# Optimization experiments

Measured on AMD Instinct MI355X. Metric: run time of the kernel, lower is better.

Reference implementation:

```python
import jax, jax.numpy as jnp
import numpy as np

N = 100000
E = 1600000
IN_FEATS = 512
N_HIDDEN = 128
N_CLASSES = 40


def setup_inputs() -> dict:
    key = jax.random.key(0)
    k1, k2, k3, k4, k5, k6, k7 = jax.random.split(key, 7)
    inputs = jax.random.normal(k1, (N, IN_FEATS), dtype=jnp.float32)
    edge_index = jax.random.randint(k2, (2, E), 0, N, dtype=jnp.int64)
    edge_attr = jax.random.uniform(k3, (E,), dtype=jnp.float32)
    # GCNConv params (Glorot-ish scaling)
    W1 = jax.random.normal(k4, (IN_FEATS, N_HIDDEN), dtype=jnp.float32) / np.sqrt(IN_FEATS)
    b1 = jnp.zeros((N_HIDDEN,), dtype=jnp.float32)
    W2 = jax.random.normal(k5, (N_HIDDEN, N_CLASSES), dtype=jnp.float32) / np.sqrt(N_HIDDEN)
    b2 = jnp.zeros((N_CLASSES,), dtype=jnp.float32)
    return {"inputs": inputs, "edge_index": edge_index, "edge_attr": edge_attr,
            "W1": W1, "b1": b1, "W2": W2, "b2": b2}


def gcn_conv(x, W, b, src, dst, edge_weight):
    """GCNConv with normalize=False: linear transform, then edge-weighted
    scatter-sum from src to dst, then bias."""
    m = x @ W                                   # [N, F_out]
    msgs = m[src] * edge_weight[:, None]        # gather + weight, [E, F_out]
    agg = jax.ops.segment_sum(msgs, dst, num_segments=x.shape[0])  # scatter-add
    return agg + b


def reference(inputs, edge_index, edge_attr, W1, b1, W2, b2):
    src, dst = edge_index[0], edge_index[1]
    h = jax.nn.relu(gcn_conv(inputs, W1, b1, src, dst, edge_attr))
    # F.dropout with training=False (eval mode) is identity -> deterministic baseline
    preds = gcn_conv(h, W2, b2, src, dst, edge_attr)
    return jax.nn.log_softmax(preds, axis=1)
```

## Files before the change

kernel.cpp:

```cpp
#include <hip/hip_runtime.h>
#include <hip/hip_bf16.h>
#include <cstdint>

#define N_NODES 100000
#define N_EDGES 1600000
#define F_IN    512
#define F_HID   128
#define F_OUT   40
#define F_OUT_PAD 48

#define BSH    8
#define NB     391
#define BEPT   8
#define BCHUNK 4096
#define GB     391
#define FCAP   6144

typedef short v8s __attribute__((ext_vector_type(8)));
typedef float v4f __attribute__((ext_vector_type(4)));

__device__ __forceinline__ short f2bf(float f) {
    unsigned u = __float_as_uint(f);
    u += 0x7fffu + ((u >> 16) & 1u);
    return (short)(u >> 16);
}

__device__ __forceinline__ v8s pack8(float4 a, float4 b) {
    v8s r;
    r[0] = f2bf(a.x); r[1] = f2bf(a.y); r[2] = f2bf(a.z); r[3] = f2bf(a.w);
    r[4] = f2bf(b.x); r[5] = f2bf(b.y); r[6] = f2bf(b.z); r[7] = f2bf(b.w);
    return r;
}

__device__ __forceinline__ void gload16(const void* g, void* l) {
    __builtin_amdgcn_global_load_lds(
        (const __attribute__((address_space(1))) void*)g,
        (__attribute__((address_space(3))) void*)l, 16, 0, 0);
}


__global__ __launch_bounds__(512) void k_bhist(const int* __restrict__ dst,
                                               int* __restrict__ bcnt) {
    __shared__ int lh[512];
    int tid = threadIdx.x;
    lh[tid] = 0;
    __syncthreads();
    long e0 = (long)blockIdx.x * BCHUNK;
#pragma unroll
    for (int i = 0; i < BEPT; i++) {
        long e = e0 + tid + i * 512;
        if (e < N_EDGES) atomicAdd(&lh[dst[e] >> BSH], 1);
    }
    __syncthreads();
    if (tid < NB && lh[tid]) atomicAdd(&bcnt[tid], lh[tid]);
}

__global__ __launch_bounds__(512) void k_bscan(const int* __restrict__ bcnt,
                                               int* __restrict__ bbase,
                                               int* __restrict__ bcur) {
    __shared__ int sm[512];
    int tid = threadIdx.x;
    int v = (tid < NB) ? bcnt[tid] : 0;
    sm[tid] = v;
    __syncthreads();
    for (int off = 1; off < 512; off <<= 1) {
        int t = (tid >= off) ? sm[tid - off] : 0;
        __syncthreads();
        sm[tid] += t;
        __syncthreads();
    }
    if (tid < NB) {
        int ex = sm[tid] - v;
        bbase[tid] = ex;
        bcur[tid] = ex;
    }
    if (tid == 511) bbase[NB] = sm[511];
}

__global__ __launch_bounds__(512) void k_bscatter(const int* __restrict__ src,
                                                  const int* __restrict__ dst,
                                                  const float* __restrict__ w,
                                                  int* __restrict__ bcur,
                                                  int2* __restrict__ tmp) {
    __shared__ int cntA[512];
    __shared__ int ofsA[512];
    __shared__ int lcur[512];
    __shared__ int gb[512];
    __shared__ __align__(16) int2 recBuf[BCHUNK];
    __shared__ unsigned short bkt[BCHUNK];
    int tid = threadIdx.x;
    long e0 = (long)blockIdx.x * BCHUNK;
    cntA[tid] = 0;
    __syncthreads();

    int dloc[BEPT];
#pragma unroll
    for (int i = 0; i < BEPT; i++) {
        long e = e0 + tid + i * 512;
        int d = (e < N_EDGES) ? dst[e] : -1;
        dloc[i] = d;
        if (d >= 0) atomicAdd(&cntA[d >> BSH], 1);
    }
    __syncthreads();

    int v = cntA[tid];
    ofsA[tid] = v;
    __syncthreads();
    for (int off = 1; off < 512; off <<= 1) {
        int t = (tid >= off) ? ofsA[tid - off] : 0;
        __syncthreads();
        ofsA[tid] += t;
        __syncthreads();
    }
    int excl = ofsA[tid] - v;
    ofsA[tid] = excl;
    lcur[tid] = excl;
    if (tid < NB && v > 0) gb[tid] = atomicAdd(&bcur[tid], v);
    __syncthreads();

#pragma unroll
    for (int i = 0; i < BEPT; i++) {
        int d = dloc[i];
        if (d >= 0) {
            long e = e0 + tid + i * 512;
            int j = d >> BSH;
            int slot = atomicAdd(&lcur[j], 1);
            recBuf[slot] = make_int2(src[e] | ((d & 255) << 17), __float_as_int(w[e]));
            bkt[slot] = (unsigned short)j;
        }
    }
    __syncthreads();

    long rem = N_EDGES - e0;
    int total = (rem < BCHUNK) ? (int)rem : BCHUNK;
    for (int s = tid; s < total; s += 512) {
        int j = bkt[s];
        tmp[gb[j] + (s - ofsA[j])] = recBuf[s];
    }
}

__global__ __launch_bounds__(256) void k_fine(const int2* __restrict__ tmp,
                                              const int* __restrict__ bbase,
                                              int2* __restrict__ rec,
                                              int* __restrict__ rowptr,
                                              int* __restrict__ deg) {
    __shared__ int hist[256];
    __shared__ int ofs[256];
    __shared__ int cur[256];
    __shared__ __align__(16) int2 recOut[FCAP];
    int tid = threadIdx.x, b = blockIdx.x;
    int base = bbase[b];
    int cnt = bbase[b + 1] - base;

    hist[tid] = 0;
    __syncthreads();
    for (int i = tid; i < cnt; i += 256) {
        unsigned u = (unsigned)tmp[base + i].x;
        atomicAdd(&hist[u >> 17], 1);
    }
    __syncthreads();

    int v = hist[tid];
    ofs[tid] = v;
    __syncthreads();
    for (int off = 1; off < 256; off <<= 1) {
        int t = (tid >= off) ? ofs[tid - off] : 0;
        __syncthreads();
        ofs[tid] += t;
        __syncthreads();
    }
    int excl = ofs[tid] - v;
    ofs[tid] = excl;
    cur[tid] = excl;
    int node = (b << BSH) + tid;
    if (node < N_NODES) {
        rowptr[node] = base + excl;
        deg[node] = v;
    }
    __syncthreads();

    if (cnt <= FCAP) {
        for (int i = tid; i < cnt; i += 256) {
            int2 r = tmp[base + i];
            unsigned u = (unsigned)r.x;
            int slot = atomicAdd(&cur[u >> 17], 1);
            recOut[slot] = make_int2((int)(u & 0x1FFFFu), r.y);
        }
        __syncthreads();
        for (int i = tid; i < cnt; i += 256) rec[base + i] = recOut[i];
    } else {
        for (int i = tid; i < cnt; i += 256) {
            int2 r = tmp[base + i];
            unsigned u = (unsigned)r.x;
            int slot = atomicAdd(&cur[u >> 17], 1);
            rec[base + slot] = make_int2((int)(u & 0x1FFFFu), r.y);
        }
    }
}


__global__ void k_convW(const float* __restrict__ W1, short* __restrict__ WT1,
                        const float* __restrict__ W2, short* __restrict__ WT2) {
    int i = blockIdx.x * blockDim.x + threadIdx.x;
    if (i < F_IN * F_HID) {
        int n = i >> 9, k = i & 511;
        WT1[i] = f2bf(W1[k * F_HID + n]);
    } else {
        int j = i - F_IN * F_HID;
        if (j < F_OUT_PAD * F_HID) {
            int n = j >> 7, k = j & 127;
            WT2[j] = (n < F_OUT) ? f2bf(W2[k * F_OUT + n]) : (short)0;
        }
    }
}


__global__ __launch_bounds__(256) void k_gemm1(const float* __restrict__ x,
                                               const short* __restrict__ WT1,
                                               unsigned short* __restrict__ m1b) {
    __shared__ __align__(16) float aBuf[2][64 * 32];
    __shared__ __align__(16) short bBuf[2][128 * 32];
    int tid = threadIdx.x, w = tid >> 6, lane = tid & 63;
    int quad = lane >> 4, l16 = lane & 15;
    long rowBase = (long)blockIdx.x * 64;

    int ar = lane >> 3, ac = lane & 7;
    int br = lane >> 2, bc = lane & 3;

    v4f acc[8];
#pragma unroll
    for (int t = 0; t < 8; t++) acc[t] = (v4f){0.f, 0.f, 0.f, 0.f};

    auto stage = [&](int kc, int buf) {
#pragma unroll
        for (int i = 0; i < 2; i++) {
            int rl = w * 16 + i * 8 + ar;
            long rg = rowBase + rl;
            if (rg > N_NODES - 1) rg = N_NODES - 1;
            const float* gp = x + rg * F_IN + kc * 32 + ((ac ^ (rl & 7)) << 2);
            gload16(gp, &aBuf[buf][(w * 16 + i * 8) * 32]);
        }
#pragma unroll
        for (int i = 0; i < 2; i++) {
            int n = w * 32 + i * 16 + br;
            const short* gp = WT1 + n * F_IN + kc * 32 + ((bc ^ ((n >> 1) & 3)) << 3);
            gload16(gp, &bBuf[buf][(w * 32 + i * 16) * 32]);
        }
    };

    stage(0, 0);
#pragma unroll
    for (int kc = 0; kc < 16; kc++) {
        __syncthreads();
        int buf = kc & 1;
        if (kc < 15) stage(kc + 1, buf ^ 1);
        int arow = w * 16 + l16;
        int p0 = (2 * quad) ^ (l16 & 7);
        float4 av0 = *(const float4*)&aBuf[buf][arow * 32 + p0 * 4];
        float4 av1 = *(const float4*)&aBuf[buf][arow * 32 + (p0 ^ 1) * 4];
        v8s af = pack8(av0, av1);
#pragma unroll
        for (int t = 0; t < 8; t++) {
            int n = t * 16 + l16;
            int p = quad ^ ((n >> 1) & 3);
            v8s bf = *(const v8s*)&bBuf[buf][n * 32 + p * 8];
            acc[t] = __builtin_amdgcn_mfma_f32_16x16x32_bf16(af, bf, acc[t], 0, 0, 0);
        }
    }

#pragma unroll
    for (int t = 0; t < 8; t++)
#pragma unroll
        for (int r = 0; r < 4; r++) {
            long row = rowBase + w * 16 + quad * 4 + r;
            if (row < N_NODES)
                m1b[row * F_HID + t * 16 + l16] = (unsigned short)f2bf(acc[t][r]);
        }
}


__global__ void k_agg1(const int2* __restrict__ rec, const int* __restrict__ rowptr,
                       const int* __restrict__ deg, const unsigned* __restrict__ m1u,
                       const float* __restrict__ b1, unsigned* __restrict__ h) {
    int node = blockIdx.x * 4 + (threadIdx.x >> 6);
    int lane = threadIdx.x & 63;
    if (node >= N_NODES) return;
    int start = rowptr[node], cnt = deg[node];

    float ax0 = 0.f, ay0 = 0.f, ax1 = 0.f, ay1 = 0.f;
    float ax2 = 0.f, ay2 = 0.f, ax3 = 0.f, ay3 = 0.f;
    int i = 0;
    for (; i + 4 <= cnt; i += 4) {
        int2 r0 = rec[start + i + 0];
        int2 r1 = rec[start + i + 1];
        int2 r2 = rec[start + i + 2];
        int2 r3 = rec[start + i + 3];
        unsigned u0 = m1u[(long)r0.x * 64 + lane];
        unsigned u1 = m1u[(long)r1.x * 64 + lane];
        unsigned u2 = m1u[(long)r2.x * 64 + lane];
        unsigned u3 = m1u[(long)r3.x * 64 + lane];
        float w0 = __int_as_float(r0.y), w1 = __int_as_float(r1.y);
        float w2 = __int_as_float(r2.y), w3 = __int_as_float(r3.y);
        ax0 = fmaf(w0, __uint_as_float(u0 << 16), ax0);
        ay0 = fmaf(w0, __uint_as_float(u0 & 0xffff0000u), ay0);
        ax1 = fmaf(w1, __uint_as_float(u1 << 16), ax1);
        ay1 = fmaf(w1, __uint_as_float(u1 & 0xffff0000u), ay1);
        ax2 = fmaf(w2, __uint_as_float(u2 << 16), ax2);
        ay2 = fmaf(w2, __uint_as_float(u2 & 0xffff0000u), ay2);
        ax3 = fmaf(w3, __uint_as_float(u3 << 16), ax3);
        ay3 = fmaf(w3, __uint_as_float(u3 & 0xffff0000u), ay3);
    }
    for (; i < cnt; i++) {
        int2 r = rec[start + i];
        unsigned u = m1u[(long)r.x * 64 + lane];
        float w = __int_as_float(r.y);
        ax0 = fmaf(w, __uint_as_float(u << 16), ax0);
        ay0 = fmaf(w, __uint_as_float(u & 0xffff0000u), ay0);
    }
    float accx = (ax0 + ax1) + (ax2 + ax3) + b1[2 * lane];
    float accy = (ay0 + ay1) + (ay2 + ay3) + b1[2 * lane + 1];
    accx = fmaxf(accx, 0.f);
    accy = fmaxf(accy, 0.f);
    unsigned packed = (unsigned)(unsigned short)f2bf(accx) |
                      ((unsigned)(unsigned short)f2bf(accy) << 16);
    h[(long)node * 64 + lane] = packed;
}


__global__ __launch_bounds__(256) void k_gemm2(const unsigned short* __restrict__ h,
                                               const short* __restrict__ WT2,
                                               unsigned short* __restrict__ m2b) {
    int wave = threadIdx.x >> 6, lane = threadIdx.x & 63;
    int quad = lane >> 4, l16 = lane & 15;
    long rowBase = ((long)blockIdx.x * 4 + wave) * 16;
    if (rowBase >= N_NODES) return;

    v4f acc[3];
#pragma unroll
    for (int t = 0; t < 3; t++) acc[t] = (v4f){0.f, 0.f, 0.f, 0.f};

    const short* arow = (const short*)h + (rowBase + l16) * (long)F_HID + quad * 8;
    const short* brow = WT2 + l16 * F_HID + quad * 8;
#pragma unroll
    for (int k0 = 0; k0 < F_HID; k0 += 32) {
        v8s af = *reinterpret_cast<const v8s*>(arow + k0);
#pragma unroll
        for (int t = 0; t < 3; t++) {
            v8s bf = *reinterpret_cast<const v8s*>(brow + t * 16 * F_HID + k0);
            acc[t] = __builtin_amdgcn_mfma_f32_16x16x32_bf16(af, bf, acc[t], 0, 0, 0);
        }
    }
#pragma unroll
    for (int r = 0; r < 4; r++) {
        long row = rowBase + quad * 4 + r;
#pragma unroll
        for (int t = 0; t < 3; t++)
            m2b[row * 64 + t * 16 + l16] = (unsigned short)f2bf(acc[t][r]);
        m2b[row * 64 + 48 + l16] = 0;
    }
}


__global__ void k_agg2(const int2* __restrict__ rec, const int* __restrict__ rowptr,
                       const int* __restrict__ deg, const unsigned short* __restrict__ m2b,
                       const float* __restrict__ b2, float* __restrict__ out) {
    int node = blockIdx.x * 4 + (threadIdx.x >> 6);
    int lane = threadIdx.x & 63;
    if (node >= N_NODES) return;
    int start = rowptr[node], cnt = deg[node];

    float a0 = 0.f, a1 = 0.f, a2 = 0.f, a3 = 0.f;
    int i = 0;
    for (; i + 4 <= cnt; i += 4) {
        int2 r0 = rec[start + i + 0];
        int2 r1 = rec[start + i + 1];
        int2 r2 = rec[start + i + 2];
        int2 r3 = rec[start + i + 3];
        unsigned short u0 = m2b[(long)r0.x * 64 + lane];
        unsigned short u1 = m2b[(long)r1.x * 64 + lane];
        unsigned short u2 = m2b[(long)r2.x * 64 + lane];
        unsigned short u3 = m2b[(long)r3.x * 64 + lane];
        a0 = fmaf(__int_as_float(r0.y), __uint_as_float((unsigned)u0 << 16), a0);
        a1 = fmaf(__int_as_float(r1.y), __uint_as_float((unsigned)u1 << 16), a1);
        a2 = fmaf(__int_as_float(r2.y), __uint_as_float((unsigned)u2 << 16), a2);
        a3 = fmaf(__int_as_float(r3.y), __uint_as_float((unsigned)u3 << 16), a3);
    }
    for (; i < cnt; i++) {
        int2 r = rec[start + i];
        unsigned short u = m2b[(long)r.x * 64 + lane];
        a0 = fmaf(__int_as_float(r.y), __uint_as_float((unsigned)u << 16), a0);
    }
    float acc = (a0 + a1) + (a2 + a3);
    if (lane < F_OUT) acc += b2[lane];
    float p = (lane < F_OUT) ? acc : -3.4e38f;
#pragma unroll
    for (int off = 32; off; off >>= 1) p = fmaxf(p, __shfl_xor(p, off));
    float ex = (lane < F_OUT) ? __expf(acc - p) : 0.f;
    float s = ex;
#pragma unroll
    for (int off = 32; off; off >>= 1) s += __shfl_xor(s, off);
    if (lane < F_OUT) out[(long)node * F_OUT + lane] = acc - p - __logf(s);
}


extern "C" void kernel_launch(void* const* d_in, const int* in_sizes, int n_in,
                              void* d_out, int out_size, void* d_ws, size_t ws_size,
                              hipStream_t stream) {
    const float* x  = (const float*)d_in[0];
    const int* ei   = (const int*)d_in[1];
    const int* src  = ei;
    const int* dst  = ei + N_EDGES;
    const float* ew = (const float*)d_in[2];
    const float* W1 = (const float*)d_in[3];
    const float* b1 = (const float*)d_in[4];
    const float* W2 = (const float*)d_in[5];
    const float* b2 = (const float*)d_in[6];
    float* out = (float*)d_out;

    char* ws = (char*)d_ws;
    size_t off = 0;
    auto alloc = [&](size_t bytes) {
        void* p = ws + off;
        off += (bytes + 255) & ~(size_t)255;
        return p;
    };
    unsigned short* m1b  = (unsigned short*)alloc((size_t)N_NODES * F_HID * 2);
    unsigned int*   h    = (unsigned int*)alloc((size_t)N_NODES * F_HID * 2);
    unsigned short* m2b  = (unsigned short*)alloc((size_t)N_NODES * 64 * 2);
    int2*           rec  = (int2*)alloc((size_t)N_EDGES * 8);
    int*          rowptr = (int*)alloc((size_t)N_NODES * 4);
    int*          deg    = (int*)alloc((size_t)N_NODES * 4);
    int*          bCnt   = (int*)alloc(512 * 4);
    int*          bBase  = (int*)alloc(512 * 4);
    int*          bCur   = (int*)alloc(512 * 4);
    short*        WT1    = (short*)alloc((size_t)F_HID * F_IN * 2);
    short*        WT2    = (short*)alloc((size_t)F_OUT_PAD * F_HID * 2);

    int2* tmp = (int2*)m2b;

    hipMemsetAsync(bCnt, 0, 512 * 4, stream);

    int convTot = F_IN * F_HID + F_OUT_PAD * F_HID;
    k_convW<<<(convTot + 255) / 256, 256, 0, stream>>>(W1, WT1, W2, WT2);

    k_bhist<<<GB, 512, 0, stream>>>(dst, bCnt);
    k_bscan<<<1, 512, 0, stream>>>(bCnt, bBase, bCur);
    k_bscatter<<<GB, 512, 0, stream>>>(src, dst, ew, bCur, tmp);
    k_fine<<<NB, 256, 0, stream>>>(tmp, bBase, rec, rowptr, deg);

    k_gemm1<<<(N_NODES + 63) / 64, 256, 0, stream>>>(x, WT1, m1b);
    k_agg1<<<(N_NODES + 3) / 4, 256, 0, stream>>>(rec, rowptr, deg, (const unsigned*)m1b, b1, h);
    k_gemm2<<<(N_NODES + 63) / 64, 256, 0, stream>>>((const unsigned short*)h, WT2, m2b);
    k_agg2<<<(N_NODES + 3) / 4, 256, 0, stream>>>(rec, rowptr, deg, m2b, b2, out);
}
```

Measured before the change: 523.1 us.

## Split aggregation wavefronts across edges with wider gathers and fuse weight conversion

```diff
diff --git a/kernel.cpp b/kernel.cpp
--- a/kernel.cpp
+++ b/kernel.cpp
@@ -14,6 +14,7 @@
 #define BEPT   8
 #define BCHUNK 4096
 #define GB     391
+#define CONVB  140
 #define FCAP   6144
 
 typedef short v8s __attribute__((ext_vector_type(8)));
@@ -24,6 +25,9 @@
     u += 0x7fffu + ((u >> 16) & 1u);
     return (short)(u >> 16);
 }
+
+__device__ __forceinline__ float bflo(unsigned u) { return __uint_as_float(u << 16); }
+__device__ __forceinline__ float bfhi(unsigned u) { return __uint_as_float(u & 0xffff0000u); }
 
 __device__ __forceinline__ v8s pack8(float4 a, float4 b) {
     v8s r;
@@ -40,7 +44,25 @@
 
 
 __global__ __launch_bounds__(512) void k_bhist(const int* __restrict__ dst,
-                                               int* __restrict__ bcnt) {
+                                               int* __restrict__ bcnt,
+                                               const float* __restrict__ W1,
+                                               short* __restrict__ WT1,
+                                               const float* __restrict__ W2,
+                                               short* __restrict__ WT2) {
+    if (blockIdx.x >= GB) {
+        int i = (blockIdx.x - GB) * 512 + threadIdx.x;
+        if (i < F_IN * F_HID) {
+            int n = i >> 9, k = i & 511;
+            WT1[i] = f2bf(W1[k * F_HID + n]);
+        } else {
+            int j = i - F_IN * F_HID;
+            if (j < F_OUT_PAD * F_HID) {
+                int n = j >> 7, k = j & 127;
+                WT2[j] = (n < F_OUT) ? f2bf(W2[k * F_OUT + n]) : (short)0;
+            }
+        }
+        return;
+    }
     __shared__ int lh[512];
     int tid = threadIdx.x;
     lh[tid] = 0;
@@ -199,22 +221,6 @@
 }
 
 
-__global__ void k_convW(const float* __restrict__ W1, short* __restrict__ WT1,
-                        const float* __restrict__ W2, short* __restrict__ WT2) {
-    int i = blockIdx.x * blockDim.x + threadIdx.x;
-    if (i < F_IN * F_HID) {
-        int n = i >> 9, k = i & 511;
-        WT1[i] = f2bf(W1[k * F_HID + n]);
-    } else {
-        int j = i - F_IN * F_HID;
-        if (j < F_OUT_PAD * F_HID) {
-            int n = j >> 7, k = j & 127;
-            WT2[j] = (n < F_OUT) ? f2bf(W2[k * F_OUT + n]) : (short)0;
-        }
-    }
-}
-
-
 __global__ __launch_bounds__(256) void k_gemm1(const float* __restrict__ x,
                                                const short* __restrict__ WT1,
                                                unsigned short* __restrict__ m1b) {
@@ -280,50 +286,64 @@
 
 
 __global__ void k_agg1(const int2* __restrict__ rec, const int* __restrict__ rowptr,
-                       const int* __restrict__ deg, const unsigned* __restrict__ m1u,
-                       const float* __restrict__ b1, unsigned* __restrict__ h) {
+                       const int* __restrict__ deg, const uint2* __restrict__ m1v,
+                       const float* __restrict__ b1, uint2* __restrict__ h2) {
     int node = blockIdx.x * 4 + (threadIdx.x >> 6);
     int lane = threadIdx.x & 63;
     if (node >= N_NODES) return;
+    int half = lane >> 5, l32 = lane & 31;
     int start = rowptr[node], cnt = deg[node];
 
-    float ax0 = 0.f, ay0 = 0.f, ax1 = 0.f, ay1 = 0.f;
-    float ax2 = 0.f, ay2 = 0.f, ax3 = 0.f, ay3 = 0.f;
-    int i = 0;
-    for (; i + 4 <= cnt; i += 4) {
-        int2 r0 = rec[start + i + 0];
-        int2 r1 = rec[start + i + 1];
-        int2 r2 = rec[start + i + 2];
-        int2 r3 = rec[start + i + 3];
-        unsigned u0 = m1u[(long)r0.x * 64 + lane];
-        unsigned u1 = m1u[(long)r1.x * 64 + lane];
-        unsigned u2 = m1u[(long)r2.x * 64 + lane];
-        unsigned u3 = m1u[(long)r3.x * 64 + lane];
+    float a0 = 0.f, a1 = 0.f, a2 = 0.f, a3 = 0.f;
+    float c0 = 0.f, c1 = 0.f, c2 = 0.f, c3 = 0.f;
+
+    int nmain = cnt >> 3;
+    int ebase = start + half;
+    for (int k = 0; k < nmain; k++) {
+        int e = ebase + (k << 3);
+        int2 r0 = rec[e];
+        int2 r1 = rec[e + 2];
+        int2 r2 = rec[e + 4];
+        int2 r3 = rec[e + 6];
+        uint2 g0 = m1v[(long)r0.x * 32 + l32];
+        uint2 g1 = m1v[(long)r1.x * 32 + l32];
+        uint2 g2 = m1v[(long)r2.x * 32 + l32];
+        uint2 g3 = m1v[(long)r3.x * 32 + l32];
         float w0 = __int_as_float(r0.y), w1 = __int_as_float(r1.y);
         float w2 = __int_as_float(r2.y), w3 = __int_as_float(r3.y);
-        ax0 = fmaf(w0, __uint_as_float(u0 << 16), ax0);
-        ay0 = fmaf(w0, __uint_as_float(u0 & 0xffff0000u), ay0);
-        ax1 = fmaf(w1, __uint_as_float(u1 << 16), ax1);
-        ay1 = fmaf(w1, __uint_as_float(u1 & 0xffff0000u), ay1);
-        ax2 = fmaf(w2, __uint_as_float(u2 << 16), ax2);
-        ay2 = fmaf(w2, __uint_as_float(u2 & 0xffff0000u), ay2);
-        ax3 = fmaf(w3, __uint_as_float(u3 << 16), ax3);
-        ay3 = fmaf(w3, __uint_as_float(u3 & 0xffff0000u), ay3);
-    }
-    for (; i < cnt; i++) {
-        int2 r = rec[start + i];
-        unsigned u = m1u[(long)r.x * 64 + lane];
+        a0 = fmaf(w0, bflo(g0.x), a0); a1 = fmaf(w0, bfhi(g0.x), a1);
+        a2 = fmaf(w0, bflo(g0.y), a2); a3 = fmaf(w0, bfhi(g0.y), a3);
+        c0 = fmaf(w1, bflo(g1.x), c0); c1 = fmaf(w1, bfhi(g1.x), c1);
+        c2 = fmaf(w1, bflo(g1.y), c2); c3 = fmaf(w1, bfhi(g1.y), c3);
+        a0 = fmaf(w2, bflo(g2.x), a0); a1 = fmaf(w2, bfhi(g2.x), a1);
+        a2 = fmaf(w2, bflo(g2.y), a2); a3 = fmaf(w2, bfhi(g2.y), a3);
+        c0 = fmaf(w3, bflo(g3.x), c0); c1 = fmaf(w3, bfhi(g3.x), c1);
+        c2 = fmaf(w3, bflo(g3.y), c2); c3 = fmaf(w3, bfhi(g3.y), c3);
+    }
+    for (int e = start + (nmain << 3) + half; e < start + cnt; e += 2) {
+        int2 r = rec[e];
+        uint2 g = m1v[(long)r.x * 32 + l32];
         float w = __int_as_float(r.y);
-        ax0 = fmaf(w, __uint_as_float(u << 16), ax0);
-        ay0 = fmaf(w, __uint_as_float(u & 0xffff0000u), ay0);
-    }
-    float accx = (ax0 + ax1) + (ax2 + ax3) + b1[2 * lane];
-    float accy = (ay0 + ay1) + (ay2 + ay3) + b1[2 * lane + 1];
-    accx = fmaxf(accx, 0.f);
-    accy = fmaxf(accy, 0.f);
-    unsigned packed = (unsigned)(unsigned short)f2bf(accx) |
-                      ((unsigned)(unsigned short)f2bf(accy) << 16);
-    h[(long)node * 64 + lane] = packed;
+        a0 = fmaf(w, bflo(g.x), a0); a1 = fmaf(w, bfhi(g.x), a1);
+        a2 = fmaf(w, bflo(g.y), a2); a3 = fmaf(w, bfhi(g.y), a3);
+    }
+    a0 += c0; a1 += c1; a2 += c2; a3 += c3;
+    a0 += __shfl_xor(a0, 32);
+    a1 += __shfl_xor(a1, 32);
+    a2 += __shfl_xor(a2, 32);
+    a3 += __shfl_xor(a3, 32);
+    if (half == 0) {
+        float4 bv = ((const float4*)b1)[l32];
+        a0 = fmaxf(a0 + bv.x, 0.f);
+        a1 = fmaxf(a1 + bv.y, 0.f);
+        a2 = fmaxf(a2 + bv.z, 0.f);
+        a3 = fmaxf(a3 + bv.w, 0.f);
+        unsigned lo = (unsigned)(unsigned short)f2bf(a0) |
+                      ((unsigned)(unsigned short)f2bf(a1) << 16);
+        unsigned hi = (unsigned)(unsigned short)f2bf(a2) |
+                      ((unsigned)(unsigned short)f2bf(a3) << 16);
+        h2[(long)node * 32 + l32] = make_uint2(lo, hi);
+    }
 }
 
 
@@ -362,44 +382,64 @@
 
 
 __global__ void k_agg2(const int2* __restrict__ rec, const int* __restrict__ rowptr,
-                       const int* __restrict__ deg, const unsigned short* __restrict__ m2b,
+                       const int* __restrict__ deg, const uint2* __restrict__ m2v,
                        const float* __restrict__ b2, float* __restrict__ out) {
     int node = blockIdx.x * 4 + (threadIdx.x >> 6);
     int lane = threadIdx.x & 63;
     if (node >= N_NODES) return;
+    int q = lane >> 4, l16 = lane & 15;
     int start = rowptr[node], cnt = deg[node];
 
     float a0 = 0.f, a1 = 0.f, a2 = 0.f, a3 = 0.f;
-    int i = 0;
-    for (; i + 4 <= cnt; i += 4) {
-        int2 r0 = rec[start + i + 0];
-        int2 r1 = rec[start + i + 1];
-        int2 r2 = rec[start + i + 2];
-        int2 r3 = rec[start + i + 3];
-        unsigned short u0 = m2b[(long)r0.x * 64 + lane];
-        unsigned short u1 = m2b[(long)r1.x * 64 + lane];
-        unsigned short u2 = m2b[(long)r2.x * 64 + lane];
-        unsigned short u3 = m2b[(long)r3.x * 64 + lane];
-        a0 = fmaf(__int_as_float(r0.y), __uint_as_float((unsigned)u0 << 16), a0);
-        a1 = fmaf(__int_as_float(r1.y), __uint_as_float((unsigned)u1 << 16), a1);
-        a2 = fmaf(__int_as_float(r2.y), __uint_as_float((unsigned)u2 << 16), a2);
-        a3 = fmaf(__int_as_float(r3.y), __uint_as_float((unsigned)u3 << 16), a3);
-    }
-    for (; i < cnt; i++) {
-        int2 r = rec[start + i];
-        unsigned short u = m2b[(long)r.x * 64 + lane];
-        a0 = fmaf(__int_as_float(r.y), __uint_as_float((unsigned)u << 16), a0);
-    }
-    float acc = (a0 + a1) + (a2 + a3);
-    if (lane < F_OUT) acc += b2[lane];
-    float p = (lane < F_OUT) ? acc : -3.4e38f;
-#pragma unroll
-    for (int off = 32; off; off >>= 1) p = fmaxf(p, __shfl_xor(p, off));
-    float ex = (lane < F_OUT) ? __expf(acc - p) : 0.f;
-    float s = ex;
-#pragma unroll
-    for (int off = 32; off; off >>= 1) s += __shfl_xor(s, off);
-    if (lane < F_OUT) out[(long)node * F_OUT + lane] = acc - p - __logf(s);
+    float c0 = 0.f, c1 = 0.f, c2 = 0.f, c3 = 0.f;
+
+    int nmain = cnt >> 3;
+    int ebase = start + q;
+    for (int k = 0; k < nmain; k++) {
+        int e = ebase + (k << 3);
+        int2 r0 = rec[e];
+        int2 r1 = rec[e + 4];
+        uint2 g0 = m2v[(long)r0.x * 16 + l16];
+        uint2 g1 = m2v[(long)r1.x * 16 + l16];
+        float w0 = __int_as_float(r0.y), w1 = __int_as_float(r1.y);
+        a0 = fmaf(w0, bflo(g0.x), a0); a1 = fmaf(w0, bfhi(g0.x), a1);
+        a2 = fmaf(w0, bflo(g0.y), a2); a3 = fmaf(w0, bfhi(g0.y), a3);
+        c0 = fmaf(w1, bflo(g1.x), c0); c1 = fmaf(w1, bfhi(g1.x), c1);
+        c2 = fmaf(w1, bflo(g1.y), c2); c3 = fmaf(w1, bfhi(g1.y), c3);
+    }
+    for (int e = start + (nmain << 3) + q; e < start + cnt; e += 4) {
+        int2 r = rec[e];
+        uint2 g = m2v[(long)r.x * 16 + l16];
+        float w = __int_as_float(r.y);
+        a0 = fmaf(w, bflo(g.x), a0); a1 = fmaf(w, bfhi(g.x), a1);
+        a2 = fmaf(w, bflo(g.y), a2); a3 = fmaf(w, bfhi(g.y), a3);
+    }
+    a0 += c0; a1 += c1; a2 += c2; a3 += c3;
+    a0 += __shfl_xor(a0, 16); a0 += __shfl_xor(a0, 32);
+    a1 += __shfl_xor(a1, 16); a1 += __shfl_xor(a1, 32);
+    a2 += __shfl_xor(a2, 16); a2 += __shfl_xor(a2, 32);
+    a3 += __shfl_xor(a3, 16); a3 += __shfl_xor(a3, 32);
+
+    const float NEG = -3.4e38f;
+    float v0 = NEG, v1 = NEG, v2 = NEG, v3 = NEG;
+    if (l16 < 10) {
+        float4 bv = ((const float4*)b2)[l16];
+        v0 = a0 + bv.x; v1 = a1 + bv.y; v2 = a2 + bv.z; v3 = a3 + bv.w;
+    }
+    float m = fmaxf(fmaxf(v0, v1), fmaxf(v2, v3));
+#pragma unroll
+    for (int off = 1; off < 16; off <<= 1) m = fmaxf(m, __shfl_xor(m, off));
+    float s = 0.f;
+    if (l16 < 10)
+        s = __expf(v0 - m) + __expf(v1 - m) + __expf(v2 - m) + __expf(v3 - m);
+#pragma unroll
+    for (int off = 1; off < 16; off <<= 1) s += __shfl_xor(s, off);
+    if (q == 0 && l16 < 10) {
+        float ls = m + __logf(s);
+        float4 o;
+        o.x = v0 - ls; o.y = v1 - ls; o.z = v2 - ls; o.w = v3 - ls;
+        ((float4*)out)[(long)node * 10 + l16] = o;
+    }
 }
 
 
@@ -440,16 +480,15 @@
 
     hipMemsetAsync(bCnt, 0, 512 * 4, stream);
 
-    int convTot = F_IN * F_HID + F_OUT_PAD * F_HID;
-    k_convW<<<(convTot + 255) / 256, 256, 0, stream>>>(W1, WT1, W2, WT2);
-
-    k_bhist<<<GB, 512, 0, stream>>>(dst, bCnt);
+    k_bhist<<<GB + CONVB, 512, 0, stream>>>(dst, bCnt, W1, WT1, W2, WT2);
     k_bscan<<<1, 512, 0, stream>>>(bCnt, bBase, bCur);
     k_bscatter<<<GB, 512, 0, stream>>>(src, dst, ew, bCur, tmp);
     k_fine<<<NB, 256, 0, stream>>>(tmp, bBase, rec, rowptr, deg);
 
     k_gemm1<<<(N_NODES + 63) / 64, 256, 0, stream>>>(x, WT1, m1b);
-    k_agg1<<<(N_NODES + 3) / 4, 256, 0, stream>>>(rec, rowptr, deg, (const unsigned*)m1b, b1, h);
+    k_agg1<<<(N_NODES + 3) / 4, 256, 0, stream>>>(rec, rowptr, deg,
+                                                  (const uint2*)m1b, b1, (uint2*)h);
     k_gemm2<<<(N_NODES + 63) / 64, 256, 0, stream>>>((const unsigned short*)h, WT2, m2b);
-    k_agg2<<<(N_NODES + 3) / 4, 256, 0, stream>>>(rec, rowptr, deg, m2b, b2, out);
-}
+    k_agg2<<<(N_NODES + 3) / 4, 256, 0, stream>>>(rec, rowptr, deg,
+                                                  (const uint2*)m2b, b2, out);
+}
```

Result: faster. 497.6 us (-4.9%).
